# Performance work log

Measured on AMD Instinct MI355X. Metric: run time of the kernel, lower is better.

## Reference

```python
import jax, jax.numpy as jnp
import numpy as np

N_NODES = 100000


def _gcn_layer(x, W, b, src, dst, n):
    # symmetric normalization (add_self_loops=False): deg = in-degree at dst
    deg = jax.ops.segment_sum(jnp.ones_like(src, dtype=x.dtype), dst, num_segments=n)
    dis = jnp.where(deg > 0, jax.lax.rsqrt(jnp.maximum(deg, 1.0)), 0.0)
    h = x @ W                                    # [N, out]
    norm = dis[src] * dis[dst]                   # [E]
    msg = h[src] * norm[:, None]                 # [E, out]
    out = jax.ops.segment_sum(msg, dst, num_segments=n)
    return out + b


def setup_inputs() -> dict:
    key = jax.random.key(0)
    k1, k2, k3, k4, k5, k6 = jax.random.split(key, 6)
    F_IN, HID, OUT = 64, 64, 2
    x = jax.random.normal(k1, (N_NODES, F_IN), dtype=jnp.float32)
    edge_index = jax.random.randint(k2, (2, 1600000), 0, N_NODES, dtype=jnp.int64)
    s1 = 1.0 / np.sqrt(2 * F_IN)
    s2 = 1.0 / np.sqrt(HID)
    W1 = jax.random.uniform(k3, (2 * F_IN, HID), jnp.float32, -s1, s1)
    b1 = jax.random.uniform(k4, (HID,), jnp.float32, -s1, s1)
    W2 = jax.random.uniform(k5, (HID, OUT), jnp.float32, -s2, s2)
    b2 = jax.random.uniform(k6, (OUT,), jnp.float32, -s2, s2)
    return {"x": x, "edge_index": edge_index, "W1": W1, "b1": b1, "W2": W2, "b2": b2}


def reference(x, edge_index, W1, b1, W2, b2):
    n = x.shape[0]
    src, dst = edge_index[0], edge_index[1]
    # global mean pool broadcast to every node, concat on feature dim -> [N, 2F]
    mean = jnp.mean(x, axis=0, keepdims=True)
    complete = jnp.concatenate([x, jnp.broadcast_to(mean, x.shape)], axis=1)
    h = _gcn_layer(complete, W1, b1, src, dst, n)
    h = jax.nn.relu(h)
    out = _gcn_layer(h, W2, b2, src, dst, n)
    return out
```

## Files before the change

kernel.cpp:

```cpp
#include <hip/hip_runtime.h>


#define NPB        256
#define NPB_SHIFT  8
#define BKTS       512
#define BKT_CAP    5120
#define CHUNK      4096
#define EPT        8
#define CS_BLK     64
#define CUR_STRIDE 32

using bf16x8 = __attribute__((ext_vector_type(8))) short;
using f32x4  = __attribute__((ext_vector_type(4))) float;

__device__ __forceinline__ unsigned short f2bf(float v) {
    unsigned u = __float_as_uint(v);
    u += 0x7FFFu + ((u >> 16) & 1u);
    return (unsigned short)(u >> 16);
}
__device__ __forceinline__ float bfu_lo(unsigned u) { return __uint_as_float(u << 16); }
__device__ __forceinline__ float bfu_hi(unsigned u) { return __uint_as_float(u & 0xFFFF0000u); }

__global__ __launch_bounds__(512) void bucketAC_kernel(
        const int* __restrict__ src, const int* __restrict__ dst,
        int e, unsigned* __restrict__ pairs, int* __restrict__ cursor,
        const float* __restrict__ x, float* __restrict__ sums,
        const float* __restrict__ W1, unsigned short* __restrict__ wtg, int n) {
    int tid = threadIdx.x;
    if (blockIdx.x < CS_BLK) {
        __shared__ float4 s4[512];
        int cb = blockIdx.x;
        const float4* x4 = (const float4*)x;
        int total4 = n * 16;
        float4 acc = make_float4(0.f, 0.f, 0.f, 0.f);
        for (int i = cb * 512 + tid; i < total4; i += CS_BLK * 512) {
            float4 v = x4[i];
            acc.x += v.x; acc.y += v.y; acc.z += v.z; acc.w += v.w;
        }
        s4[tid] = acc;
        __syncthreads();
        if (tid < 16) {
            float4 v = s4[tid];
            for (int k = 1; k < 32; ++k) {
                float4 w = s4[tid + 16 * k];
                v.x += w.x; v.y += w.y; v.z += w.z; v.w += w.w;
            }
            atomicAdd(&sums[tid * 4 + 0], v.x);
            atomicAdd(&sums[tid * 4 + 1], v.y);
            atomicAdd(&sums[tid * 4 + 2], v.z);
            atomicAdd(&sums[tid * 4 + 3], v.w);
        }
        return;
    }
    if (blockIdx.x == CS_BLK) {
        for (int i = tid; i < 4096; i += 512) {
            int k = i >> 6, j = i & 63;
            wtg[j * 64 + k] = f2bf(W1[k * 64 + j]);
        }
        return;
    }
    __shared__ int cnt[BKTS], sb[BKTS], gpos[BKTS];
    __shared__ unsigned stage[CHUNK];
    __shared__ unsigned short bb[CHUNK];
    int chunkStart = (blockIdx.x - CS_BLK - 1) * CHUNK;
    int v = e - chunkStart;
    if (v > CHUNK) v = CHUNK;
    cnt[tid] = 0;
    __syncthreads();
    int myb[EPT], myoff[EPT];
    unsigned myp[EPT];
#pragma unroll
    for (int t = 0; t < EPT; ++t) {
        int i = chunkStart + t * 512 + tid;
        myb[t] = -1;
        if (i < e) {
            int s = src[i], d = dst[i];
            myb[t] = d >> NPB_SHIFT;
            myp[t] = ((unsigned)s << NPB_SHIFT) | (unsigned)(d & (NPB - 1));
            myoff[t] = atomicAdd(&cnt[myb[t]], 1);
        }
    }
    __syncthreads();
    sb[tid] = cnt[tid];
    __syncthreads();
    for (int off = 1; off < BKTS; off <<= 1) {
        int t = (tid >= off) ? sb[tid - off] : 0;
        __syncthreads();
        sb[tid] += t;
        __syncthreads();
    }
    {
        int excl = tid ? sb[tid - 1] : 0;
        int cb = cnt[tid];
        if (cb > 0) {
            int gb = atomicAdd(&cursor[tid * CUR_STRIDE], cb);
            gpos[tid] = tid * BKT_CAP + gb - excl;
        }
        cnt[tid] = excl;
    }
    __syncthreads();
#pragma unroll
    for (int t = 0; t < EPT; ++t) {
        if (myb[t] >= 0) {
            int p = cnt[myb[t]] + myoff[t];
            stage[p] = myp[t];
            bb[p] = (unsigned short)myb[t];
        }
    }
    __syncthreads();
    for (int j = tid; j < v; j += 512) {
        int bk = bb[j];
        int wi = gpos[bk] + j;
        if (wi < (bk + 1) * BKT_CAP) pairs[wi] = stage[j];
    }
}

__global__ __launch_bounds__(512) void csrBG_kernel(
        const unsigned* __restrict__ pairs, const int* __restrict__ cursor,
        float* __restrict__ dis, int* __restrict__ rowstart,
        int* __restrict__ eidx, int n,
        const float* __restrict__ sums, const float* __restrict__ W1,
        const unsigned short* __restrict__ wtg, const float* __restrict__ x,
        unsigned short* __restrict__ h1s) {
    __shared__ int ldeg[NPB];
    __shared__ int lcur[NPB];
    __shared__ int scanbuf[512];
    __shared__ int s_ebase;
    __shared__ __align__(16) float cv[64];
    __shared__ unsigned short Ws[64 * 72];
    __shared__ unsigned short Xs[2][64 * 72];
    float* disl = (float*)ldeg;
    int b = blockIdx.x;
    int tid = threadIdx.x;
    int node0 = b << NPB_SHIFT;
    int nl = n - node0;
    if (nl > NPB) nl = NPB;
    int cnt_b = cursor[b * CUR_STRIDE];
    if (cnt_b > BKT_CAP) cnt_b = BKT_CAP;
    if (tid < NPB) ldeg[tid] = 0;
    if (tid == 0) s_ebase = 0;
    __syncthreads();
    if (tid < b) atomicAdd(&s_ebase, cursor[tid * CUR_STRIDE]);
    const unsigned* mp = pairs + (size_t)b * BKT_CAP;
    for (int i = tid; i < cnt_b; i += 512)
        atomicAdd(&ldeg[mp[i] & (NPB - 1)], 1);
    __syncthreads();
    scanbuf[tid] = (tid < NPB) ? ldeg[tid] : 0;
    __syncthreads();
    for (int off = 1; off < 512; off <<= 1) {
        int t = (tid >= off) ? scanbuf[tid - off] : 0;
        __syncthreads();
        scanbuf[tid] += t;
        __syncthreads();
    }
    int ebase = s_ebase;
    int mydeg = 0;
    if (tid < NPB) {
        int ex = tid ? scanbuf[tid - 1] : 0;
        lcur[tid] = ex;
        mydeg = ldeg[tid];
        if (tid < nl) rowstart[node0 + tid] = ebase + ex;
    }
    if (tid == 0 && node0 + NPB >= n)
        rowstart[n] = ebase + cnt_b;
    __syncthreads();
    if (tid < NPB) {
        float dv = mydeg > 0 ? rsqrtf((float)mydeg) : 0.f;
        disl[tid] = dv;
        if (tid < nl) dis[node0 + tid] = dv;
    }
    for (int i = tid; i < cnt_b; i += 512) {
        unsigned p = mp[i];
        int pos = atomicAdd(&lcur[p & (NPB - 1)], 1);
        eidx[ebase + pos] = (int)(p >> NPB_SHIFT);
    }
    if (tid < 64) {
        float inv_n = 1.0f / (float)n;
        float acc = 0.f;
        for (int k = 0; k < 64; ++k) acc += (sums[k] * inv_n) * W1[(64 + k) * 64 + tid];
        cv[tid] = acc;
    }
    for (int i = tid; i < 1024; i += 512) {
        int j = i >> 4, k4 = (i & 15) * 4;
        *(ushort4*)&Ws[j * 72 + k4] = *(const ushort4*)&wtg[j * 64 + k4];
    }
    int lane = tid & 63;
    int wv = tid >> 6;
    int tile = wv >> 2;
    int w4 = wv & 3;
    int l15 = lane & 15;
    int quad = lane >> 4;
#pragma unroll
    for (int it = 0; it < 2; ++it) {
        __syncthreads();
        for (int i = tid; i < 2048; i += 512) {
            int r = i >> 4, k4 = (i & 15) * 4;
            int gr = node0 + it * 128 + r;
            float4 xv = make_float4(0.f, 0.f, 0.f, 0.f);
            if (gr < n) xv = *(const float4*)&x[(size_t)gr * 64 + k4];
            ushort4 hv;
            hv.x = f2bf(xv.x); hv.y = f2bf(xv.y); hv.z = f2bf(xv.z); hv.w = f2bf(xv.w);
            *(ushort4*)&Xs[r >> 6][(r & 63) * 72 + k4] = hv;
        }
        __syncthreads();
        int xrow = w4 * 16 + l15;
        f32x4 acc0 = {0.f, 0.f, 0.f, 0.f}, acc1 = acc0, acc2 = acc0, acc3 = acc0;
#pragma unroll
        for (int ks = 0; ks < 2; ++ks) {
            bf16x8 bfrag = *(const bf16x8*)&Xs[tile][xrow * 72 + ks * 32 + quad * 8];
            bf16x8 a0 = *(const bf16x8*)&Ws[(0 * 16 + l15) * 72 + ks * 32 + quad * 8];
            bf16x8 a1 = *(const bf16x8*)&Ws[(1 * 16 + l15) * 72 + ks * 32 + quad * 8];
            bf16x8 a2 = *(const bf16x8*)&Ws[(2 * 16 + l15) * 72 + ks * 32 + quad * 8];
            bf16x8 a3 = *(const bf16x8*)&Ws[(3 * 16 + l15) * 72 + ks * 32 + quad * 8];
            acc0 = __builtin_amdgcn_mfma_f32_16x16x32_bf16(a0, bfrag, acc0, 0, 0, 0);
            acc1 = __builtin_amdgcn_mfma_f32_16x16x32_bf16(a1, bfrag, acc1, 0, 0, 0);
            acc2 = __builtin_amdgcn_mfma_f32_16x16x32_bf16(a2, bfrag, acc2, 0, 0, 0);
            acc3 = __builtin_amdgcn_mfma_f32_16x16x32_bf16(a3, bfrag, acc3, 0, 0, 0);
        }
        int lrow = it * 128 + tile * 64 + xrow;
        int grow = node0 + lrow;
        if (grow < n) {
            float dv = disl[lrow];
            const float4* c4 = (const float4*)cv;
            f32x4 accs[4] = {acc0, acc1, acc2, acc3};
#pragma unroll
            for (int t = 0; t < 4; ++t) {
                float4 cj = c4[t * 4 + quad];
                ushort4 hs;
                hs.x = f2bf((accs[t][0] + cj.x) * dv);
                hs.y = f2bf((accs[t][1] + cj.y) * dv);
                hs.z = f2bf((accs[t][2] + cj.z) * dv);
                hs.w = f2bf((accs[t][3] + cj.w) * dv);
                *(ushort4*)&h1s[(size_t)grow * 64 + t * 16 + quad * 4] = hs;
            }
        }
    }
}

__global__ void gather1_kernel(const int* __restrict__ rowstart,
                               const int* __restrict__ eidx, const float* __restrict__ dis,
                               const unsigned short* __restrict__ h1s,
                               const float* __restrict__ b1, const float* __restrict__ W2,
                               float* __restrict__ h2s, int n) {
    int lane = threadIdx.x & 63;
    int node = blockIdx.x * 4 + (threadIdx.x >> 6);
    if (node >= n) return;
    int rs = rowstart[node];
    int re = rowstart[node + 1];
    int dn = re - rs;
    int m = dn < 64 ? dn : 64;
    int eHeld = (lane < m) ? eidx[rs + lane] : 0;
    int sub = lane >> 5;
    int fp  = (lane & 31) * 2;
    float ax = 0.f, ay = 0.f;
    int j = 0;
    for (; j + 16 <= m; j += 16) {
        int s0 = __shfl(eHeld, j + 0 + sub, 64);
        int s1 = __shfl(eHeld, j + 2 + sub, 64);
        int s2 = __shfl(eHeld, j + 4 + sub, 64);
        int s3 = __shfl(eHeld, j + 6 + sub, 64);
        int s4 = __shfl(eHeld, j + 8 + sub, 64);
        int s5 = __shfl(eHeld, j + 10 + sub, 64);
        int s6 = __shfl(eHeld, j + 12 + sub, 64);
        int s7 = __shfl(eHeld, j + 14 + sub, 64);
        unsigned u0 = *(const unsigned*)&h1s[((size_t)s0 << 6) + fp];
        unsigned u1 = *(const unsigned*)&h1s[((size_t)s1 << 6) + fp];
        unsigned u2 = *(const unsigned*)&h1s[((size_t)s2 << 6) + fp];
        unsigned u3 = *(const unsigned*)&h1s[((size_t)s3 << 6) + fp];
        unsigned u4 = *(const unsigned*)&h1s[((size_t)s4 << 6) + fp];
        unsigned u5 = *(const unsigned*)&h1s[((size_t)s5 << 6) + fp];
        unsigned u6 = *(const unsigned*)&h1s[((size_t)s6 << 6) + fp];
        unsigned u7 = *(const unsigned*)&h1s[((size_t)s7 << 6) + fp];
        ax += (bfu_lo(u0) + bfu_lo(u1)) + (bfu_lo(u2) + bfu_lo(u3))
            + (bfu_lo(u4) + bfu_lo(u5)) + (bfu_lo(u6) + bfu_lo(u7));
        ay += (bfu_hi(u0) + bfu_hi(u1)) + (bfu_hi(u2) + bfu_hi(u3))
            + (bfu_hi(u4) + bfu_hi(u5)) + (bfu_hi(u6) + bfu_hi(u7));
    }
    for (; j + 8 <= m; j += 8) {
        int s0 = __shfl(eHeld, j + 0 + sub, 64);
        int s1 = __shfl(eHeld, j + 2 + sub, 64);
        int s2 = __shfl(eHeld, j + 4 + sub, 64);
        int s3 = __shfl(eHeld, j + 6 + sub, 64);
        unsigned u0 = *(const unsigned*)&h1s[((size_t)s0 << 6) + fp];
        unsigned u1 = *(const unsigned*)&h1s[((size_t)s1 << 6) + fp];
        unsigned u2 = *(const unsigned*)&h1s[((size_t)s2 << 6) + fp];
        unsigned u3 = *(const unsigned*)&h1s[((size_t)s3 << 6) + fp];
        ax += (bfu_lo(u0) + bfu_lo(u1)) + (bfu_lo(u2) + bfu_lo(u3));
        ay += (bfu_hi(u0) + bfu_hi(u1)) + (bfu_hi(u2) + bfu_hi(u3));
    }
    for (; j + 4 <= m; j += 4) {
        int s0 = __shfl(eHeld, j + 0 + sub, 64);
        int s1 = __shfl(eHeld, j + 2 + sub, 64);
        unsigned u0 = *(const unsigned*)&h1s[((size_t)s0 << 6) + fp];
        unsigned u1 = *(const unsigned*)&h1s[((size_t)s1 << 6) + fp];
        ax += bfu_lo(u0) + bfu_lo(u1);
        ay += bfu_hi(u0) + bfu_hi(u1);
    }
    for (; j < m; j += 2) {
        int jj = j + sub;
        int s = __shfl(eHeld, jj < m ? jj : 0, 64);
        if (jj < m) {
            unsigned u = *(const unsigned*)&h1s[((size_t)s << 6) + fp];
            ax += bfu_lo(u);
            ay += bfu_hi(u);
        }
    }
    for (int t = 64; t < dn; ++t) {
        if (sub == 0) {
            int s = eidx[rs + t];
            unsigned u = *(const unsigned*)&h1s[((size_t)s << 6) + fp];
            ax += bfu_lo(u);
            ay += bfu_hi(u);
        }
    }
    ax += __shfl_xor(ax, 32, 64);
    ay += __shfl_xor(ay, 32, 64);
    float di = dis[node];
    float2 bv = ((const float2*)b1)[lane & 31];
    float4 w = ((const float4*)W2)[lane & 31];
    float t0 = fmaxf(di * ax + bv.x, 0.f);
    float t1 = fmaxf(di * ay + bv.y, 0.f);
    float v0 = t0 * w.x + t1 * w.z;
    float v1 = t0 * w.y + t1 * w.w;
#pragma unroll
    for (int off = 1; off <= 16; off <<= 1) {
        v0 += __shfl_xor(v0, off, 64);
        v1 += __shfl_xor(v1, off, 64);
    }
    if (lane == 0) {
        h2s[(size_t)node * 2 + 0] = di * v0;
        h2s[(size_t)node * 2 + 1] = di * v1;
    }
}

__global__ void gather2_kernel(const int* __restrict__ rowstart,
                               const int* __restrict__ eidx, const float* __restrict__ dis,
                               const float2* __restrict__ h2s, const float* __restrict__ b2,
                               float2* __restrict__ out, int n) {
    int tid = threadIdx.x;
    int node = blockIdx.x * 16 + (tid >> 4);
    if (node >= n) return;
    int el = tid & 15;
    int rs = rowstart[node];
    int dn = rowstart[node + 1] - rs;
    float ax = 0.f, ay = 0.f;
    for (int t = el; t < dn; t += 16) {
        int s = eidx[rs + t];
        float2 h = h2s[s];
        ax += h.x;
        ay += h.y;
    }
#pragma unroll
    for (int off = 1; off <= 8; off <<= 1) {
        ax += __shfl_xor(ax, off, 64);
        ay += __shfl_xor(ay, off, 64);
    }
    if (el == 0) {
        float di = dis[node];
        out[node] = make_float2(di * ax + b2[0], di * ay + b2[1]);
    }
}

extern "C" void kernel_launch(void* const* d_in, const int* in_sizes, int n_in,
                              void* d_out, int out_size, void* d_ws, size_t ws_size,
                              hipStream_t stream) {
    const float* x  = (const float*)d_in[0];
    const int*   ei = (const int*)d_in[1];
    const float* W1 = (const float*)d_in[2];
    const float* b1 = (const float*)d_in[3];
    const float* W2 = (const float*)d_in[4];
    const float* b2 = (const float*)d_in[5];
    float2* out = (float2*)d_out;

    const int n = in_sizes[0] / 64;
    const int e = in_sizes[1] / 2;
    const int* srcI = ei;
    const int* dstI = ei + e;
    const int nbkt = (n + NPB - 1) >> NPB_SHIFT;

    char* p = (char*)d_ws;
    int* rowstart = (int*)p;    p += ((size_t)(n + 1) * 4 + 255) & ~255ull;
    float* dis    = (float*)p;  p += ((size_t)n * 4 + 255) & ~255ull;
    float* sums   = (float*)p;
    int* cursor   = (int*)(p + 256);
    size_t zsize  = 256 + (size_t)nbkt * CUR_STRIDE * 4;
    char* zbase   = p;          p += (zsize + 255) & ~255ull;
    unsigned short* wtg = (unsigned short*)p;  p += (4096 * 2 + 255) & ~255ull;
    int* eidx     = (int*)p;    p += ((size_t)e * 4 + 255) & ~255ull;
    unsigned* pairs = (unsigned*)p;  p += ((size_t)nbkt * BKT_CAP * 4 + 255) & ~255ull;
    unsigned short* h1s = (unsigned short*)p;  p += ((size_t)n * 64 * 2 + 255) & ~255ull;
    float* h2s    = (float*)p;

    hipMemsetAsync(zbase, 0, zsize, stream);

    const int nchunks = (e + CHUNK - 1) / CHUNK;

    bucketAC_kernel<<<CS_BLK + 1 + nchunks, 512, 0, stream>>>(srcI, dstI, e, pairs, cursor,
                                                              x, sums, W1, wtg, n);
    csrBG_kernel<<<nbkt, 512, 0, stream>>>(pairs, cursor, dis, rowstart, eidx, n,
                                           sums, W1, wtg, x, h1s);
    gather1_kernel<<<(n + 3) / 4, 256, 0, stream>>>(rowstart, eidx, dis, h1s, b1, W2, h2s, n);
    gather2_kernel<<<(n + 15) / 16, 256, 0, stream>>>(rowstart, eidx, dis, (const float2*)h2s,
                                                      b2, out, n);
}
```

Measured before the change: 185.7 us.

## Move column-mean into GEMM stage and apply mean term during first gather

Drops the separate column-sum and weight-transpose blocks from the bucketing kernel. The column sum is now taken from the bf16-staged X tile inside the CSR/GEMM kernel via atomics. Because the mean term now exists only after that kernel, its projection is computed per node in gather1 and added as dis-weighted neighbour sum times c. The aim is to avoid a second full read of x, but gather1 now does a 64-iteration dot product per wavefront and extra dis gathers, and the mean is summed from bf16-rounded values.

```diff
diff --git a/kernel.cpp b/kernel.cpp
--- a/kernel.cpp
+++ b/kernel.cpp
@@ -7,7 +7,6 @@
 #define BKT_CAP    5120
 #define CHUNK      4096
 #define EPT        8
-#define CS_BLK     64
 #define CUR_STRIDE 32
 
 using bf16x8 = __attribute__((ext_vector_type(8))) short;
@@ -18,51 +17,20 @@
     u += 0x7FFFu + ((u >> 16) & 1u);
     return (unsigned short)(u >> 16);
 }
+__device__ __forceinline__ float bf2f(unsigned short h) {
+    return __uint_as_float((unsigned)h << 16);
+}
 __device__ __forceinline__ float bfu_lo(unsigned u) { return __uint_as_float(u << 16); }
 __device__ __forceinline__ float bfu_hi(unsigned u) { return __uint_as_float(u & 0xFFFF0000u); }
 
-__global__ __launch_bounds__(512) void bucketAC_kernel(
+__global__ __launch_bounds__(512) void bucketA_kernel(
         const int* __restrict__ src, const int* __restrict__ dst,
-        int e, unsigned* __restrict__ pairs, int* __restrict__ cursor,
-        const float* __restrict__ x, float* __restrict__ sums,
-        const float* __restrict__ W1, unsigned short* __restrict__ wtg, int n) {
-    int tid = threadIdx.x;
-    if (blockIdx.x < CS_BLK) {
-        __shared__ float4 s4[512];
-        int cb = blockIdx.x;
-        const float4* x4 = (const float4*)x;
-        int total4 = n * 16;
-        float4 acc = make_float4(0.f, 0.f, 0.f, 0.f);
-        for (int i = cb * 512 + tid; i < total4; i += CS_BLK * 512) {
-            float4 v = x4[i];
-            acc.x += v.x; acc.y += v.y; acc.z += v.z; acc.w += v.w;
-        }
-        s4[tid] = acc;
-        __syncthreads();
-        if (tid < 16) {
-            float4 v = s4[tid];
-            for (int k = 1; k < 32; ++k) {
-                float4 w = s4[tid + 16 * k];
-                v.x += w.x; v.y += w.y; v.z += w.z; v.w += w.w;
-            }
-            atomicAdd(&sums[tid * 4 + 0], v.x);
-            atomicAdd(&sums[tid * 4 + 1], v.y);
-            atomicAdd(&sums[tid * 4 + 2], v.z);
-            atomicAdd(&sums[tid * 4 + 3], v.w);
-        }
-        return;
-    }
-    if (blockIdx.x == CS_BLK) {
-        for (int i = tid; i < 4096; i += 512) {
-            int k = i >> 6, j = i & 63;
-            wtg[j * 64 + k] = f2bf(W1[k * 64 + j]);
-        }
-        return;
-    }
+        int e, unsigned* __restrict__ pairs, int* __restrict__ cursor) {
     __shared__ int cnt[BKTS], sb[BKTS], gpos[BKTS];
     __shared__ unsigned stage[CHUNK];
     __shared__ unsigned short bb[CHUNK];
-    int chunkStart = (blockIdx.x - CS_BLK - 1) * CHUNK;
+    int tid = threadIdx.x;
+    int chunkStart = blockIdx.x * CHUNK;
     int v = e - chunkStart;
     if (v > CHUNK) v = CHUNK;
     cnt[tid] = 0;
@@ -119,20 +87,19 @@
         const unsigned* __restrict__ pairs, const int* __restrict__ cursor,
         float* __restrict__ dis, int* __restrict__ rowstart,
         int* __restrict__ eidx, int n,
-        const float* __restrict__ sums, const float* __restrict__ W1,
-        const unsigned short* __restrict__ wtg, const float* __restrict__ x,
-        unsigned short* __restrict__ h1s) {
+        const float* __restrict__ W1, const float* __restrict__ x,
+        unsigned short* __restrict__ h1s, float* __restrict__ sums) {
     __shared__ int ldeg[NPB];
     __shared__ int lcur[NPB];
     __shared__ int scanbuf[512];
     __shared__ int s_ebase;
-    __shared__ __align__(16) float cv[64];
     __shared__ unsigned short Ws[64 * 72];
     __shared__ unsigned short Xs[2][64 * 72];
     float* disl = (float*)ldeg;
     int b = blockIdx.x;
     int tid = threadIdx.x;
     int node0 = b << NPB_SHIFT;
+    if (node0 >= n) return;
     int nl = n - node0;
     if (nl > NPB) nl = NPB;
     int cnt_b = cursor[b * CUR_STRIDE];
@@ -174,15 +141,9 @@
         int pos = atomicAdd(&lcur[p & (NPB - 1)], 1);
         eidx[ebase + pos] = (int)(p >> NPB_SHIFT);
     }
-    if (tid < 64) {
-        float inv_n = 1.0f / (float)n;
-        float acc = 0.f;
-        for (int k = 0; k < 64; ++k) acc += (sums[k] * inv_n) * W1[(64 + k) * 64 + tid];
-        cv[tid] = acc;
-    }
-    for (int i = tid; i < 1024; i += 512) {
-        int j = i >> 4, k4 = (i & 15) * 4;
-        *(ushort4*)&Ws[j * 72 + k4] = *(const ushort4*)&wtg[j * 64 + k4];
+    for (int i = tid; i < 4096; i += 512) {
+        int k = i >> 6, j = i & 63;
+        Ws[j * 72 + k] = f2bf(W1[i]);
     }
     int lane = tid & 63;
     int wv = tid >> 6;
@@ -203,6 +164,16 @@
             *(ushort4*)&Xs[r >> 6][(r & 63) * 72 + k4] = hv;
         }
         __syncthreads();
+        {
+            int cj = tid & 63;
+            int r0 = (tid >> 6) * 16;
+            int ct = r0 >> 6;
+            float ps = 0.f;
+#pragma unroll
+            for (int rr = 0; rr < 16; ++rr)
+                ps += bf2f(Xs[ct][((r0 + rr) & 63) * 72 + cj]);
+            atomicAdd(&sums[cj], ps);
+        }
         int xrow = w4 * 16 + l15;
         f32x4 acc0 = {0.f, 0.f, 0.f, 0.f}, acc1 = acc0, acc2 = acc0, acc3 = acc0;
 #pragma unroll
@@ -221,16 +192,14 @@
         int grow = node0 + lrow;
         if (grow < n) {
             float dv = disl[lrow];
-            const float4* c4 = (const float4*)cv;
             f32x4 accs[4] = {acc0, acc1, acc2, acc3};
 #pragma unroll
             for (int t = 0; t < 4; ++t) {
-                float4 cj = c4[t * 4 + quad];
                 ushort4 hs;
-                hs.x = f2bf((accs[t][0] + cj.x) * dv);
-                hs.y = f2bf((accs[t][1] + cj.y) * dv);
-                hs.z = f2bf((accs[t][2] + cj.z) * dv);
-                hs.w = f2bf((accs[t][3] + cj.w) * dv);
+                hs.x = f2bf(accs[t][0] * dv);
+                hs.y = f2bf(accs[t][1] * dv);
+                hs.z = f2bf(accs[t][2] * dv);
+                hs.w = f2bf(accs[t][3] * dv);
                 *(ushort4*)&h1s[(size_t)grow * 64 + t * 16 + quad * 4] = hs;
             }
         }
@@ -241,17 +210,28 @@
                                const int* __restrict__ eidx, const float* __restrict__ dis,
                                const unsigned short* __restrict__ h1s,
                                const float* __restrict__ b1, const float* __restrict__ W2,
+                               const float* __restrict__ sums, const float* __restrict__ W1,
                                float* __restrict__ h2s, int n) {
     int lane = threadIdx.x & 63;
     int node = blockIdx.x * 4 + (threadIdx.x >> 6);
     if (node >= n) return;
+    int sub = lane >> 5;
+    int fp  = (lane & 31) * 2;
+    float c0 = 0.f, c1 = 0.f;
+    for (int k = 0; k < 64; ++k) {
+        float sk = sums[k];
+        float2 wr = *(const float2*)&W1[(64 + k) * 64 + fp];
+        c0 += sk * wr.x;
+        c1 += sk * wr.y;
+    }
+    float inv_n = 1.0f / (float)n;
+    c0 *= inv_n; c1 *= inv_n;
     int rs = rowstart[node];
     int re = rowstart[node + 1];
     int dn = re - rs;
     int m = dn < 64 ? dn : 64;
     int eHeld = (lane < m) ? eidx[rs + lane] : 0;
-    int sub = lane >> 5;
-    int fp  = (lane & 31) * 2;
+    float qv = (lane < m) ? dis[eHeld] : 0.f;
     float ax = 0.f, ay = 0.f;
     int j = 0;
     for (; j + 16 <= m; j += 16) {
@@ -311,15 +291,18 @@
             unsigned u = *(const unsigned*)&h1s[((size_t)s << 6) + fp];
             ax += bfu_lo(u);
             ay += bfu_hi(u);
+            if (lane == 0) qv += dis[s];
         }
     }
     ax += __shfl_xor(ax, 32, 64);
     ay += __shfl_xor(ay, 32, 64);
+#pragma unroll
+    for (int off = 1; off <= 32; off <<= 1) qv += __shfl_xor(qv, off, 64);
     float di = dis[node];
     float2 bv = ((const float2*)b1)[lane & 31];
     float4 w = ((const float4*)W2)[lane & 31];
-    float t0 = fmaxf(di * ax + bv.x, 0.f);
-    float t1 = fmaxf(di * ay + bv.y, 0.f);
+    float t0 = fmaxf(di * (ax + qv * c0) + bv.x, 0.f);
+    float t1 = fmaxf(di * (ay + qv * c1) + bv.y, 0.f);
     float v0 = t0 * w.x + t1 * w.z;
     float v1 = t0 * w.y + t1 * w.w;
 #pragma unroll
@@ -385,7 +368,6 @@
     int* cursor   = (int*)(p + 256);
     size_t zsize  = 256 + (size_t)nbkt * CUR_STRIDE * 4;
     char* zbase   = p;          p += (zsize + 255) & ~255ull;
-    unsigned short* wtg = (unsigned short*)p;  p += (4096 * 2 + 255) & ~255ull;
     int* eidx     = (int*)p;    p += ((size_t)e * 4 + 255) & ~255ull;
     unsigned* pairs = (unsigned*)p;  p += ((size_t)nbkt * BKT_CAP * 4 + 255) & ~255ull;
     unsigned short* h1s = (unsigned short*)p;  p += ((size_t)n * 64 * 2 + 255) & ~255ull;
@@ -395,11 +377,11 @@
 
     const int nchunks = (e + CHUNK - 1) / CHUNK;
 
-    bucketAC_kernel<<<CS_BLK + 1 + nchunks, 512, 0, stream>>>(srcI, dstI, e, pairs, cursor,
-                                                              x, sums, W1, wtg, n);
+    bucketA_kernel<<<nchunks, 512, 0, stream>>>(srcI, dstI, e, pairs, cursor);
     csrBG_kernel<<<nbkt, 512, 0, stream>>>(pairs, cursor, dis, rowstart, eidx, n,
-                                           sums, W1, wtg, x, h1s);
-    gather1_kernel<<<(n + 3) / 4, 256, 0, stream>>>(rowstart, eidx, dis, h1s, b1, W2, h2s, n);
+                                           W1, x, h1s, sums);
+    gather1_kernel<<<(n + 3) / 4, 256, 0, stream>>>(rowstart, eidx, dis, h1s, b1, W2,
+                                                    sums, W1, h2s, n);
     gather2_kernel<<<(n + 15) / 16, 256, 0, stream>>>(rowstart, eidx, dis, (const float2*)h2s,
                                                       b2, out, n);
 }
```

New measurement: 473.0 us. 2.55x slower.
